# Performance work log

Measured on AMD Instinct MI355X. Metric: run time of the kernel, lower is better.

The kernel has to match this reference:

```python
import jax, jax.numpy as jnp
import numpy as np

N, E, L, F, HID, OUT = 20000, 200000, 5, 4, 128, 3


def _lin(x, w, b):
    # torch Linear convention: w is [out, in]
    return x @ w.T + b


def setup_inputs() -> dict:
    key = jax.random.key(0)
    ks = iter(jax.random.split(key, 40))
    nrm = lambda shape, s=0.05: jax.random.normal(next(ks), shape, dtype=jnp.float32) * s
    inp = {
        'x': jax.random.normal(next(ks), (N, L, F), dtype=jnp.float32),
        'edge_index': jax.random.randint(next(ks), (2, E), 0, N, dtype=jnp.int64),
        'edge_attr': jax.random.normal(next(ks), (E, F), dtype=jnp.float32),
        'batch': jnp.zeros((N,), dtype=jnp.int64),
        'node_type': jax.random.normal(next(ks), (N, 1), dtype=jnp.float32),
        # PastStateEncoder params
        'emb': nrm((L, F), 1.0),
        'conv_w': nrm((HID, 2 * F, 3)),  # Conv1d(8,128,3) OIW
        'conv_b': nrm((HID,)),
        # FusionLayer Linear(129,128)
        'fuse_w': nrm((HID, HID + 1)), 'fuse_b': nrm((HID,)),
        # gnn1 EdgeModel: Linear(2*128+4,128), Linear(128,128)
        'g1e_w1': nrm((HID, 2 * HID + F)), 'g1e_b1': nrm((HID,)),
        'g1e_w2': nrm((HID, HID)), 'g1e_b2': nrm((HID,)),
        # gnn1 NodeModel: Linear(256,128), Linear(128,128)
        'g1n_w1': nrm((HID, 2 * HID)), 'g1n_b1': nrm((HID,)),
        'g1n_w2': nrm((HID, HID)), 'g1n_b2': nrm((HID,)),
        # gnn2 EdgeModel: Linear(2*128+128,128), Linear(128,128)
        'g2e_w1': nrm((HID, 3 * HID)), 'g2e_b1': nrm((HID,)),
        'g2e_w2': nrm((HID, HID)), 'g2e_b2': nrm((HID,)),
        # gnn2 NodeModel
        'g2n_w1': nrm((HID, 2 * HID)), 'g2n_b1': nrm((HID,)),
        'g2n_w2': nrm((HID, HID)), 'g2n_b2': nrm((HID,)),
        # final_mlp: Linear(128,128), BN(128), Linear(128,3)
        'fm_w1': nrm((HID, HID)), 'fm_b1': nrm((HID,)),
        'bn_g': jnp.ones((HID,), dtype=jnp.float32), 'bn_b': jnp.zeros((HID,), dtype=jnp.float32),
        'fm_w2': nrm((OUT, HID)), 'fm_b2': nrm((OUT,)),
    }
    return inp


def _encoder(x, emb, conv_w, conv_b):
    # x: [N, L, F]; append learned positional embedding -> [N, L, 2F]
    n = x.shape[0]
    xe = jnp.concatenate([x, jnp.broadcast_to(emb[None], (n, L, F))], axis=-1)
    xc = xe.transpose(0, 2, 1)  # [N, 2F, L]
    y = jax.lax.conv_general_dilated(
        xc, conv_w, window_strides=(1,), padding=[(1, 1)],
        dimension_numbers=('NCW', 'OIW', 'NCW'))
    y = y + conv_b[None, :, None]
    return y.mean(axis=-1)  # [N, HID]


def _edge_mlp(src, dst, ea, w1, b1, w2, b2):
    h = jax.nn.relu(_lin(jnp.concatenate([src, dst, ea], axis=1), w1, b1))
    return _lin(h, w2, b2)


def _node_mlp(x_row, ea, w1, b1, w2, b2):
    h = jax.nn.relu(_lin(jnp.concatenate([x_row, ea], axis=1), w1, b1))
    return _lin(h, w2, b2)


def reference(x, edge_index, edge_attr, batch, node_type,
              emb, conv_w, conv_b, fuse_w, fuse_b,
              g1e_w1, g1e_b1, g1e_w2, g1e_b2, g1n_w1, g1n_b1, g1n_w2, g1n_b2,
              g2e_w1, g2e_b1, g2e_w2, g2e_b2, g2n_w1, g2n_b1, g2n_w2, g2n_b2,
              fm_w1, fm_b1, bn_g, bn_b, fm_w2, fm_b2):
    row, col = edge_index[0], edge_index[1]
    h = _encoder(x, emb, conv_w, conv_b)                     # [N,128]
    h = _lin(jnp.concatenate([h, node_type], axis=-1), fuse_w, fuse_b)  # [N,128]
    # gnn1 (MetaLayer: edge model then node model; node model here is per-edge)
    ea = _edge_mlp(h[row], h[col], edge_attr, g1e_w1, g1e_b1, g1e_w2, g1e_b2)  # [E,128]
    h = _node_mlp(h[row], ea, g1n_w1, g1n_b1, g1n_w2, g1n_b2)                  # [E,128]
    # gnn2 (h now lives on edges; indices < N <= E remain valid, matching torch)
    ea = _edge_mlp(h[row], h[col], ea, g2e_w1, g2e_b1, g2e_w2, g2e_b2)
    h = _node_mlp(h[row], ea, g2n_w1, g2n_b1, g2n_w2, g2n_b2)
    # final head on edge_attr: Linear -> BatchNorm1d (training stats) -> ReLU -> Linear
    z = _lin(ea, fm_w1, fm_b1)
    mu = z.mean(axis=0)
    var = z.var(axis=0)  # biased, matches torch BN normalization
    z = (z - mu) * jax.lax.rsqrt(var + 1e-5) * bn_g + bn_b
    z = jax.nn.relu(z)
    return _lin(z, fm_w2, fm_b2)  # [E,3]
```

## Files before the change

kernel.cpp:

```cpp
#include <hip/hip_runtime.h>

#define N_NODES 20000
#define N_EDGES 200000
#define HID 128
#define STR 136
#define NBLK 3125

typedef unsigned short u16;
using bf16x8 = __attribute__((ext_vector_type(8))) __bf16;
using f32x4  = __attribute__((ext_vector_type(4))) float;

__device__ __forceinline__ u16 f2bf(float f) {
  union { float f; unsigned u; } v; v.f = f;
  unsigned u = v.u;
  return (u16)((u + 0x7FFFu + ((u >> 16) & 1u)) >> 16);
}
__device__ __forceinline__ float bf2f(unsigned s) {
  union { unsigned u; float f; } v; v.u = s << 16;
  return v.f;
}
__device__ __forceinline__ bf16x8 ld8(const u16* p) { return *(const bf16x8*)p; }

__device__ __forceinline__ void zero_acc(f32x4 acc[4][2]) {
#pragma unroll
  for (int i = 0; i < 4; ++i) {
    acc[i][0] = (f32x4){0.f, 0.f, 0.f, 0.f};
    acc[i][1] = (f32x4){0.f, 0.f, 0.f, 0.f};
  }
}

template <int KSTEPS, typename AF>
__device__ __forceinline__ void wgemm(const u16* __restrict__ PW, AF afrag,
                                      f32x4 acc[4][2], int lane, int wave) {
  const u16* pb = PW + (wave * 2 * 64 + lane) * 8;
  bf16x8 b0[2], b1[2];
  b0[0] = ld8(pb);
  b1[0] = ld8(pb + 512);
#pragma unroll
  for (int ks = 0; ks < KSTEPS; ++ks) {
    const int cur = ks & 1, nxt = cur ^ 1;
    if (ks + 1 < KSTEPS) {
      b0[nxt] = ld8(pb + (ks + 1) * 4096);
      b1[nxt] = ld8(pb + (ks + 1) * 4096 + 512);
    }
#pragma unroll
    for (int mt = 0; mt < 4; ++mt) {
      bf16x8 a = afrag(ks, mt);
      acc[mt][0] = __builtin_amdgcn_mfma_f32_16x16x32_bf16(a, b0[cur], acc[mt][0], 0, 0, 0);
      acc[mt][1] = __builtin_amdgcn_mfma_f32_16x16x32_bf16(a, b1[cur], acc[mt][1], 0, 0, 0);
    }
  }
}

template <bool RELU>
__device__ __forceinline__ void epi_store(u16* buf, const f32x4 acc[4][2],
                                          const float* __restrict__ bias,
                                          int lane, int wave) {
  const int c = lane & 15, q = lane >> 4;
  const float bb0 = bias[wave * 32 + c], bb1 = bias[wave * 32 + 16 + c];
#pragma unroll
  for (int mt = 0; mt < 4; ++mt)
#pragma unroll
    for (int nt = 0; nt < 2; ++nt) {
      const float bb = nt ? bb1 : bb0;
      const int col = wave * 32 + nt * 16 + c;
#pragma unroll
      for (int r = 0; r < 4; ++r) {
        float v = acc[mt][nt][r] + bb;
        if (RELU) v = fmaxf(v, 0.f);
        buf[(mt * 16 + q * 4 + r) * STR + col] = f2bf(v);
      }
    }
}

__device__ __forceinline__ void flush_buf(const u16* buf, u16* __restrict__ gout,
                                          int e0, int tid) {
#pragma unroll
  for (int it = 0; it < 4; ++it) {
    int cid = tid + it * 256, e = cid >> 4, p = cid & 15;
    uint4 v = *(const uint4*)(buf + e * STR + p * 8);
    *(uint4*)(gout + (size_t)(e0 + e) * HID + p * 8) = v;
  }
}

__global__ void k_fold(const float* __restrict__ emb, const float* __restrict__ conv_w,
                       const float* __restrict__ conv_b, const float* __restrict__ fuse_w,
                       const float* __restrict__ fuse_b, float* __restrict__ Mt,
                       float* __restrict__ C0, float* __restrict__ Wnt) {
  __shared__ float Ash[128][21];
  int o = threadIdx.x;
  {
    float b0 = conv_b[o];
#pragma unroll
    for (int p = 0; p < 5; ++p) {
#pragma unroll
      for (int i = 0; i < 8; ++i) {
        float s = 0.f;
#pragma unroll
        for (int k = 0; k < 3; ++k) {
          int t = p + 1 - k;
          if (t >= 0 && t < 5) s += conv_w[(o * 8 + i) * 3 + k];
        }
        s *= 0.2f;
        if (i < 4) Ash[o][p * 4 + i] = s;
        else b0 += emb[p * 4 + (i - 4)] * s;
      }
    }
    Ash[o][20] = b0;
  }
  __syncthreads();
  float m[20];
#pragma unroll
  for (int qq = 0; qq < 20; ++qq) m[qq] = 0.f;
  float c0 = fuse_b[o];
  for (int j = 0; j < 128; ++j) {
    float w = fuse_w[o * 129 + j];
#pragma unroll
    for (int qq = 0; qq < 20; ++qq) m[qq] += w * Ash[j][qq];
    c0 += w * Ash[j][20];
  }
#pragma unroll
  for (int qq = 0; qq < 20; ++qq) Mt[qq * 128 + o] = m[qq];
  C0[o] = c0;
  Wnt[o] = fuse_w[o * 129 + 128];
}

struct PackArgs {
  const float* src[7];
  u16* dst[7];
  int Kin[7];
  int ksCum[8];
};

__global__ void k_pack(PackArgs pa) {
  int bk = blockIdx.x;
  int mi = 0;
  while (bk >= pa.ksCum[mi + 1]) ++mi;
  int ks = bk - pa.ksCum[mi];
  const float* W = pa.src[mi];
  u16* D = pa.dst[mi] + ks * 4096;
  int Kin = pa.Kin[mi];
#pragma unroll
  for (int t = 0; t < 16; ++t) {
    int el = t * 256 + (int)threadIdx.x;
    int j = el & 7, ln = (el >> 3) & 63, ntile = el >> 9;
    int k = ks * 32 + ((ln >> 4) << 3) + j;
    int n = ntile * 16 + (ln & 15);
    float v = (k < Kin) ? W[n * Kin + k] : 0.0f;
    D[el] = f2bf(v);
  }
}

__global__ __launch_bounds__(256) void k_encode(const float* __restrict__ x,
                                                const float* __restrict__ node_type,
                                                const float* __restrict__ Mt,
                                                const float* __restrict__ C0,
                                                const float* __restrict__ Wnt,
                                                u16* __restrict__ h2) {
  __shared__ float xs[2][20];
  int local = threadIdx.x >> 7, o = threadIdx.x & 127;
  int node = blockIdx.x * 2 + local;
  if (threadIdx.x < 40) {
    int nn = threadIdx.x / 20, qq = threadIdx.x % 20;
    xs[nn][qq] = x[(blockIdx.x * 2 + nn) * 20 + qq];
  }
  __syncthreads();
  float acc = C0[o] + Wnt[o] * node_type[node];
#pragma unroll
  for (int qq = 0; qq < 20; ++qq) acc += xs[local][qq] * Mt[qq * 128 + o];
  h2[node * HID + o] = f2bf(acc);
}

__global__ __launch_bounds__(256, 3) void k_gnn1(
    const int* __restrict__ eidx, const float* __restrict__ eattr,
    const u16* __restrict__ h2, const u16* __restrict__ pW1, const u16* __restrict__ pW2,
    const u16* __restrict__ pW3, const u16* __restrict__ pW4, const float* __restrict__ b1,
    const float* __restrict__ b2, const float* __restrict__ b3, const float* __restrict__ b4,
    u16* __restrict__ ea1, u16* __restrict__ h3) {
  __shared__ __align__(16) u16 B0[64 * STR], B1[64 * STR], B2[64 * STR];
  const int tid = threadIdx.x, lane = tid & 63, wave = tid >> 6;
  const int e0 = blockIdx.x * 64;
  const int* rowI = eidx;
  const int* colI = eidx + N_EDGES;
  const int idr = rowI[e0 + lane], idc = colI[e0 + lane];
  const u16* hrow = h2 + (size_t)idr * HID;
  const u16* hcol = h2 + (size_t)idc * HID;

#pragma unroll
  for (int it = 0; it < 8; ++it) {
    int g = wave * 8 + it;
    int p = g & 15;
    uint4 v = *(const uint4*)((g < 16 ? hrow : hcol) + p * 8);
    *(uint4*)((g < 16 ? B0 : B1) + lane * STR + p * 8) = v;
  }

  const int m = lane & 15, q = lane >> 4;
  bf16x8 ef[4];
#pragma unroll
  for (int mt = 0; mt < 4; ++mt) {
    union { u16 s[8]; uint4 u; bf16x8 v; } t;
    t.u = make_uint4(0u, 0u, 0u, 0u);
    if (q == 0) {
      float4 a = *(const float4*)(eattr + (size_t)(e0 + mt * 16 + m) * 4);
      t.s[0] = f2bf(a.x); t.s[1] = f2bf(a.y); t.s[2] = f2bf(a.z); t.s[3] = f2bf(a.w);
    }
    ef[mt] = t.v;
  }
  __syncthreads();

  const int aoff = m * STR + q * 8;
  f32x4 acc[4][2];

  zero_acc(acc);
  wgemm<9>(pW1, [&](int ks, int mt) -> bf16x8 {
    if (ks < 4) return ld8(B0 + aoff + mt * 16 * STR + ks * 32);
    if (ks < 8) return ld8(B1 + aoff + mt * 16 * STR + (ks - 4) * 32);
    return ef[mt];
  }, acc, lane, wave);
  epi_store<true>(B2, acc, b1, lane, wave);
  __syncthreads();

  zero_acc(acc);
  wgemm<4>(pW2, [&](int ks, int mt) -> bf16x8 {
    return ld8(B2 + aoff + mt * 16 * STR + ks * 32);
  }, acc, lane, wave);
  epi_store<false>(B1, acc, b2, lane, wave);
  __syncthreads();
  flush_buf(B1, ea1, e0, tid);

  if (e0 < N_NODES) {
    zero_acc(acc);
    wgemm<8>(pW3, [&](int ks, int mt) -> bf16x8 {
      if (ks < 4) return ld8(B0 + aoff + mt * 16 * STR + ks * 32);
      return ld8(B1 + aoff + mt * 16 * STR + (ks - 4) * 32);
    }, acc, lane, wave);
    epi_store<true>(B2, acc, b3, lane, wave);
    __syncthreads();
    zero_acc(acc);
    wgemm<4>(pW4, [&](int ks, int mt) -> bf16x8 {
      return ld8(B2 + aoff + mt * 16 * STR + ks * 32);
    }, acc, lane, wave);
    epi_store<false>(B0, acc, b4, lane, wave);
    __syncthreads();
    flush_buf(B0, h3, e0, tid);
  }
}

__global__ __launch_bounds__(256, 3) void k_gnn2(
    const int* __restrict__ eidx, const u16* __restrict__ h3, u16* ea1z,
    const u16* __restrict__ pW5, const u16* __restrict__ pW6, const u16* __restrict__ pW7,
    const float* __restrict__ b5, const float* __restrict__ b6, const float* __restrict__ b7,
    float* __restrict__ partials) {
  __shared__ __align__(16) u16 B0[64 * STR], B1[64 * STR], B2[64 * STR];
  const int tid = threadIdx.x, lane = tid & 63, wave = tid >> 6;
  const int e0 = blockIdx.x * 64;
  const int* rowI = eidx;
  const int* colI = eidx + N_EDGES;
  const int idr = rowI[e0 + lane], idc = colI[e0 + lane];
  const u16* hrow = h3 + (size_t)idr * HID;
  const u16* hcol = h3 + (size_t)idc * HID;

#pragma unroll
  for (int it = 0; it < 8; ++it) {
    int g = wave * 8 + it;
    int p = g & 15;
    uint4 v = *(const uint4*)((g < 16 ? hrow : hcol) + p * 8);
    *(uint4*)((g < 16 ? B0 : B1) + lane * STR + p * 8) = v;
  }
#pragma unroll
  for (int it = 0; it < 4; ++it) {
    int cid = tid + it * 256, e = cid >> 4, p = cid & 15;
    uint4 v = *(const uint4*)(ea1z + (size_t)(e0 + e) * HID + p * 8);
    *(uint4*)(B2 + e * STR + p * 8) = v;
  }
  __syncthreads();

  const int m = lane & 15, q = lane >> 4;
  const int aoff = m * STR + q * 8;
  f32x4 acc[4][2];

  zero_acc(acc);
  wgemm<12>(pW5, [&](int ks, int mt) -> bf16x8 {
    if (ks < 4) return ld8(B0 + aoff + mt * 16 * STR + ks * 32);
    if (ks < 8) return ld8(B1 + aoff + mt * 16 * STR + (ks - 4) * 32);
    return ld8(B2 + aoff + mt * 16 * STR + (ks - 8) * 32);
  }, acc, lane, wave);
  __syncthreads();
  epi_store<true>(B0, acc, b5, lane, wave);
  __syncthreads();

  zero_acc(acc);
  wgemm<4>(pW6, [&](int ks, int mt) -> bf16x8 {
    return ld8(B0 + aoff + mt * 16 * STR + ks * 32);
  }, acc, lane, wave);
  epi_store<false>(B1, acc, b6, lane, wave);
  __syncthreads();

  zero_acc(acc);
  wgemm<4>(pW7, [&](int ks, int mt) -> bf16x8 {
    return ld8(B1 + aoff + mt * 16 * STR + ks * 32);
  }, acc, lane, wave);

  {
    const int c = lane & 15;
    const float bb0 = b7[wave * 32 + c], bb1 = b7[wave * 32 + 16 + c];
    float s0 = 0.f, q0 = 0.f, s1 = 0.f, q1 = 0.f;
#pragma unroll
    for (int mt = 0; mt < 4; ++mt)
#pragma unroll
      for (int r = 0; r < 4; ++r) {
        float v0 = acc[mt][0][r] + bb0;
        float v1 = acc[mt][1][r] + bb1;
        s0 += v0; q0 += v0 * v0;
        s1 += v1; q1 += v1 * v1;
        int row = mt * 16 + q * 4 + r;
        B2[row * STR + wave * 32 + c] = f2bf(v0);
        B2[row * STR + wave * 32 + 16 + c] = f2bf(v1);
      }
    s0 += __shfl_xor(s0, 16); s0 += __shfl_xor(s0, 32);
    q0 += __shfl_xor(q0, 16); q0 += __shfl_xor(q0, 32);
    s1 += __shfl_xor(s1, 16); s1 += __shfl_xor(s1, 32);
    q1 += __shfl_xor(q1, 16); q1 += __shfl_xor(q1, 32);
    if (lane < 16) {
      int base = blockIdx.x * 256;
      partials[base + wave * 32 + lane] = s0;
      partials[base + wave * 32 + 16 + lane] = s1;
      partials[base + 128 + wave * 32 + lane] = q0;
      partials[base + 128 + wave * 32 + 16 + lane] = q1;
    }
  }
  __syncthreads();
  flush_buf(B2, ea1z, e0, tid);
}

__global__ void k_reduce(const float* __restrict__ partials, float* __restrict__ bnacc) {
  int t = threadIdx.x;
  float s = 0.f;
  for (int b = blockIdx.x; b < NBLK; b += 64) s += partials[b * 256 + t];
  atomicAdd(&bnacc[t], s);
}

__global__ void k_bnfin(const float* __restrict__ bnacc, const float* __restrict__ bn_g,
                        const float* __restrict__ bn_b, float* __restrict__ ss) {
  int t = threadIdx.x;
  float inv = 1.0f / (float)N_EDGES;
  float mu = bnacc[t] * inv;
  float var = bnacc[128 + t] * inv - mu * mu;
  float sc = bn_g[t] * rsqrtf(var + 1e-5f);
  ss[t] = sc;
  ss[128 + t] = bn_b[t] - mu * sc;
}

__global__ __launch_bounds__(256) void k_head(const u16* __restrict__ z,
                                              const float* __restrict__ ss,
                                              const float* __restrict__ w2,
                                              const float* __restrict__ b2,
                                              float* __restrict__ out) {
  __shared__ float sh_s[128], sh_h[128], sh_w0[128], sh_w1[128], sh_w2[128];
  const int tid = threadIdx.x;
  if (tid < 128) {
    sh_s[tid] = ss[tid];
    sh_h[tid] = ss[128 + tid];
    sh_w0[tid] = w2[tid];
    sh_w1[tid] = w2[128 + tid];
    sh_w2[tid] = w2[256 + tid];
  }
  __syncthreads();
  const int e = blockIdx.x * 256 + tid;
  if (e >= N_EDGES) return;
  float a0 = b2[0], a1 = b2[1], a2 = b2[2];
  const u16* zr = z + (size_t)e * HID;
#pragma unroll
  for (int p = 0; p < 16; ++p) {
    uint4 v = *(const uint4*)(zr + p * 8);
    unsigned wv[4] = {v.x, v.y, v.z, v.w};
#pragma unroll
    for (int k = 0; k < 4; ++k) {
      int ch = p * 8 + k * 2;
      float lo = bf2f(wv[k] & 0xffffu), hi = bf2f(wv[k] >> 16);
      float r0 = fmaxf(fmaf(lo, sh_s[ch], sh_h[ch]), 0.f);
      float r1 = fmaxf(fmaf(hi, sh_s[ch + 1], sh_h[ch + 1]), 0.f);
      a0 += r0 * sh_w0[ch] + r1 * sh_w0[ch + 1];
      a1 += r0 * sh_w1[ch] + r1 * sh_w1[ch + 1];
      a2 += r0 * sh_w2[ch] + r1 * sh_w2[ch + 1];
    }
  }
  out[e * 3 + 0] = a0;
  out[e * 3 + 1] = a1;
  out[e * 3 + 2] = a2;
}

extern "C" void kernel_launch(void* const* d_in, const int* in_sizes, int n_in,
                              void* d_out, int out_size, void* d_ws, size_t ws_size,
                              hipStream_t stream) {
  const float* x         = (const float*)d_in[0];
  const int* eidx        = (const int*)d_in[1];
  const float* eattr     = (const float*)d_in[2];
  const float* node_type = (const float*)d_in[4];
  const float* emb       = (const float*)d_in[5];
  const float* conv_w    = (const float*)d_in[6];
  const float* conv_b    = (const float*)d_in[7];
  const float* fuse_w    = (const float*)d_in[8];
  const float* fuse_b    = (const float*)d_in[9];
  const float* g1e_w1    = (const float*)d_in[10];
  const float* g1e_b1    = (const float*)d_in[11];
  const float* g1e_w2    = (const float*)d_in[12];
  const float* g1e_b2    = (const float*)d_in[13];
  const float* g1n_w1    = (const float*)d_in[14];
  const float* g1n_b1    = (const float*)d_in[15];
  const float* g1n_w2    = (const float*)d_in[16];
  const float* g1n_b2    = (const float*)d_in[17];
  const float* g2e_w1    = (const float*)d_in[18];
  const float* g2e_b1    = (const float*)d_in[19];
  const float* g2e_w2    = (const float*)d_in[20];
  const float* g2e_b2    = (const float*)d_in[21];
  const float* fm_w1     = (const float*)d_in[26];
  const float* fm_b1     = (const float*)d_in[27];
  const float* bn_g      = (const float*)d_in[28];
  const float* bn_b      = (const float*)d_in[29];
  const float* fm_w2     = (const float*)d_in[30];
  const float* fm_b2     = (const float*)d_in[31];
  float* out = (float*)d_out;

  char* ws = (char*)d_ws;
  size_t off = 0;
  auto take = [&](size_t bytes) {
    void* p = ws + off;
    off = (off + bytes + 255) & ~(size_t)255;
    return p;
  };
  u16* h2   = (u16*)take((size_t)N_NODES * HID * 2);
  u16* h3   = (u16*)take((size_t)20032 * HID * 2);
  u16* ea1z = (u16*)take((size_t)N_EDGES * HID * 2);
  float* Mt    = (float*)take(20 * 128 * 4);
  float* C0    = (float*)take(128 * 4);
  float* Wnt   = (float*)take(128 * 4);
  float* bnacc = (float*)take(256 * 4);
  float* bnss  = (float*)take(256 * 4);
  float* partials = (float*)take((size_t)NBLK * 256 * 4);
  u16* pW1 = (u16*)take(9 * 4096 * 2);
  u16* pW2 = (u16*)take(4 * 4096 * 2);
  u16* pW3 = (u16*)take(8 * 4096 * 2);
  u16* pW4 = (u16*)take(4 * 4096 * 2);
  u16* pW5 = (u16*)take(12 * 4096 * 2);
  u16* pW6 = (u16*)take(4 * 4096 * 2);
  u16* pW7 = (u16*)take(4 * 4096 * 2);

  hipMemsetAsync(bnacc, 0, 256 * 4, stream);
  k_fold<<<1, 128, 0, stream>>>(emb, conv_w, conv_b, fuse_w, fuse_b, Mt, C0, Wnt);

  PackArgs pa;
  const float* srcs[7] = {g1e_w1, g1e_w2, g1n_w1, g1n_w2, g2e_w1, g2e_w2, fm_w1};
  u16* dsts[7] = {pW1, pW2, pW3, pW4, pW5, pW6, pW7};
  int kins[7] = {260, 128, 256, 128, 384, 128, 128};
  int kst[7] = {9, 4, 8, 4, 12, 4, 4};
  int cum = 0;
  for (int i = 0; i < 7; ++i) {
    pa.src[i] = srcs[i]; pa.dst[i] = dsts[i]; pa.Kin[i] = kins[i];
    pa.ksCum[i] = cum; cum += kst[i];
  }
  pa.ksCum[7] = cum;
  k_pack<<<45, 256, 0, stream>>>(pa);

  k_encode<<<N_NODES / 2, 256, 0, stream>>>(x, node_type, Mt, C0, Wnt, h2);
  k_gnn1<<<NBLK, 256, 0, stream>>>(eidx, eattr, h2, pW1, pW2, pW3, pW4,
                                   g1e_b1, g1e_b2, g1n_b1, g1n_b2, ea1z, h3);
  k_gnn2<<<NBLK, 256, 0, stream>>>(eidx, h3, ea1z, pW5, pW6, pW7,
                                   g2e_b1, g2e_b2, fm_b1, partials);
  k_reduce<<<64, 256, 0, stream>>>(partials, bnacc);
  k_bnfin<<<1, 128, 0, stream>>>(bnacc, bn_g, bn_b, bnss);
  k_head<<<(N_EDGES + 255) / 256, 256, 0, stream>>>(ea1z, bnss, fm_w2, fm_b2, out);
}
```

Baseline: 288.3 us.

## Make GNN kernels persistent with register prefetch and fold final linear pair

Both GNN edge kernels become persistent: a fixed grid of 768 blocks loops over 64-edge tiles and prefetches the next tile's gathered node rows, edge attributes and indices into registers while the current tile's GEMMs run. In gnn2 the second edge-MLP linear and the head's first linear have no nonlinearity between them, so they are folded on device into one 128x128 weight. This removes one GEMM stage and one LDS round trip per tile. BN partial sums are accumulated across tiles per block, which shrinks the partials buffer and the reduce work. The cost is higher register pressure from the prefetch buffers, extra barriers per tile, and a small rounding change from the folded weight.

```diff
diff --git a/kernel.cpp b/kernel.cpp
--- a/kernel.cpp
+++ b/kernel.cpp
@@ -4,7 +4,8 @@
 #define N_EDGES 200000
 #define HID 128
 #define STR 136
-#define NBLK 3125
+#define NT 3125
+#define GPERS 768
 
 typedef unsigned short u16;
 using bf16x8 = __attribute__((ext_vector_type(8))) __bf16;
@@ -125,11 +126,26 @@
   Wnt[o] = fuse_w[o * 129 + 128];
 }
 
+__global__ void k_fold2(const float* __restrict__ w6, const float* __restrict__ b6,
+                        const float* __restrict__ w7, const float* __restrict__ b7,
+                        float* __restrict__ W67, float* __restrict__ b67) {
+  int o = blockIdx.x;
+  int k = threadIdx.x;
+  float s = 0.f;
+  for (int j = 0; j < 128; ++j) s += w7[o * 128 + j] * w6[j * 128 + k];
+  W67[o * 128 + k] = s;
+  if (k == 0) {
+    float sb = 0.f;
+    for (int j = 0; j < 128; ++j) sb += w7[o * 128 + j] * b6[j];
+    b67[o] = sb + b7[o];
+  }
+}
+
 struct PackArgs {
-  const float* src[7];
-  u16* dst[7];
-  int Kin[7];
-  int ksCum[8];
+  const float* src[6];
+  u16* dst[6];
+  int Kin[6];
+  int ksCum[7];
 };
 
 __global__ void k_pack(PackArgs pa) {
@@ -179,164 +195,221 @@
     u16* __restrict__ ea1, u16* __restrict__ h3) {
   __shared__ __align__(16) u16 B0[64 * STR], B1[64 * STR], B2[64 * STR];
   const int tid = threadIdx.x, lane = tid & 63, wave = tid >> 6;
-  const int e0 = blockIdx.x * 64;
+  const int m = lane & 15, q = lane >> 4;
+  const int aoff = m * STR + q * 8;
   const int* rowI = eidx;
   const int* colI = eidx + N_EDGES;
-  const int idr = rowI[e0 + lane], idc = colI[e0 + lane];
-  const u16* hrow = h2 + (size_t)idr * HID;
-  const u16* hcol = h2 + (size_t)idc * HID;
-
-#pragma unroll
-  for (int it = 0; it < 8; ++it) {
-    int g = wave * 8 + it;
-    int p = g & 15;
-    uint4 v = *(const uint4*)((g < 16 ? hrow : hcol) + p * 8);
-    *(uint4*)((g < 16 ? B0 : B1) + lane * STR + p * 8) = v;
-  }
-
-  const int m = lane & 15, q = lane >> 4;
-  bf16x8 ef[4];
-#pragma unroll
-  for (int mt = 0; mt < 4; ++mt) {
-    union { u16 s[8]; uint4 u; bf16x8 v; } t;
-    t.u = make_uint4(0u, 0u, 0u, 0u);
+  const int G = gridDim.x;
+
+  uint4 st[8];
+  float4 ea[4];
+  int t = blockIdx.x;
+  {
+    const int ir = rowI[t * 64 + lane], ic = colI[t * 64 + lane];
+    const u16* hr = h2 + (size_t)ir * HID;
+    const u16* hc = h2 + (size_t)ic * HID;
+#pragma unroll
+    for (int it = 0; it < 8; ++it) {
+      int g = wave * 8 + it, p = g & 15;
+      st[it] = *(const uint4*)((g < 16 ? hr : hc) + p * 8);
+    }
     if (q == 0) {
-      float4 a = *(const float4*)(eattr + (size_t)(e0 + mt * 16 + m) * 4);
-      t.s[0] = f2bf(a.x); t.s[1] = f2bf(a.y); t.s[2] = f2bf(a.z); t.s[3] = f2bf(a.w);
-    }
-    ef[mt] = t.v;
-  }
-  __syncthreads();
-
-  const int aoff = m * STR + q * 8;
+#pragma unroll
+      for (int mt = 0; mt < 4; ++mt)
+        ea[mt] = *(const float4*)(eattr + (size_t)(t * 64 + mt * 16 + m) * 4);
+    }
+  }
+
   f32x4 acc[4][2];
-
-  zero_acc(acc);
-  wgemm<9>(pW1, [&](int ks, int mt) -> bf16x8 {
-    if (ks < 4) return ld8(B0 + aoff + mt * 16 * STR + ks * 32);
-    if (ks < 8) return ld8(B1 + aoff + mt * 16 * STR + (ks - 4) * 32);
-    return ef[mt];
-  }, acc, lane, wave);
-  epi_store<true>(B2, acc, b1, lane, wave);
-  __syncthreads();
-
-  zero_acc(acc);
-  wgemm<4>(pW2, [&](int ks, int mt) -> bf16x8 {
-    return ld8(B2 + aoff + mt * 16 * STR + ks * 32);
-  }, acc, lane, wave);
-  epi_store<false>(B1, acc, b2, lane, wave);
-  __syncthreads();
-  flush_buf(B1, ea1, e0, tid);
-
-  if (e0 < N_NODES) {
+  for (; t < NT; t += G) {
+    const int e0 = t * 64;
+    const int tc = (t + G < NT) ? (t + G) : t;
+#pragma unroll
+    for (int it = 0; it < 8; ++it) {
+      int g = wave * 8 + it, p = g & 15;
+      *(uint4*)((g < 16 ? B0 : B1) + lane * STR + p * 8) = st[it];
+    }
+    bf16x8 ef[4];
+#pragma unroll
+    for (int mt = 0; mt < 4; ++mt) {
+      union { u16 s[8]; uint4 u; bf16x8 v; } tt;
+      tt.u = make_uint4(0u, 0u, 0u, 0u);
+      if (q == 0) {
+        tt.s[0] = f2bf(ea[mt].x); tt.s[1] = f2bf(ea[mt].y);
+        tt.s[2] = f2bf(ea[mt].z); tt.s[3] = f2bf(ea[mt].w);
+      }
+      ef[mt] = tt.v;
+    }
+    const int irn = rowI[tc * 64 + lane], icn = colI[tc * 64 + lane];
+    __syncthreads();
+
     zero_acc(acc);
-    wgemm<8>(pW3, [&](int ks, int mt) -> bf16x8 {
+    wgemm<9>(pW1, [&](int ks, int mt) -> bf16x8 {
       if (ks < 4) return ld8(B0 + aoff + mt * 16 * STR + ks * 32);
-      return ld8(B1 + aoff + mt * 16 * STR + (ks - 4) * 32);
+      if (ks < 8) return ld8(B1 + aoff + mt * 16 * STR + (ks - 4) * 32);
+      return ef[mt];
     }, acc, lane, wave);
-    epi_store<true>(B2, acc, b3, lane, wave);
-    __syncthreads();
+    epi_store<true>(B2, acc, b1, lane, wave);
+    if (q == 0) {
+#pragma unroll
+      for (int mt = 0; mt < 4; ++mt)
+        ea[mt] = *(const float4*)(eattr + (size_t)(tc * 64 + mt * 16 + m) * 4);
+    }
+    __syncthreads();
+
     zero_acc(acc);
-    wgemm<4>(pW4, [&](int ks, int mt) -> bf16x8 {
+    wgemm<4>(pW2, [&](int ks, int mt) -> bf16x8 {
       return ld8(B2 + aoff + mt * 16 * STR + ks * 32);
     }, acc, lane, wave);
-    epi_store<false>(B0, acc, b4, lane, wave);
-    __syncthreads();
-    flush_buf(B0, h3, e0, tid);
+    {
+      const u16* hr = h2 + (size_t)irn * HID;
+      const u16* hc = h2 + (size_t)icn * HID;
+#pragma unroll
+      for (int it = 0; it < 8; ++it) {
+        int g = wave * 8 + it, p = g & 15;
+        st[it] = *(const uint4*)((g < 16 ? hr : hc) + p * 8);
+      }
+    }
+    epi_store<false>(B1, acc, b2, lane, wave);
+    __syncthreads();
+    flush_buf(B1, ea1, e0, tid);
+
+    if (e0 < N_NODES) {
+      zero_acc(acc);
+      wgemm<8>(pW3, [&](int ks, int mt) -> bf16x8 {
+        if (ks < 4) return ld8(B0 + aoff + mt * 16 * STR + ks * 32);
+        return ld8(B1 + aoff + mt * 16 * STR + (ks - 4) * 32);
+      }, acc, lane, wave);
+      epi_store<true>(B2, acc, b3, lane, wave);
+      __syncthreads();
+      zero_acc(acc);
+      wgemm<4>(pW4, [&](int ks, int mt) -> bf16x8 {
+        return ld8(B2 + aoff + mt * 16 * STR + ks * 32);
+      }, acc, lane, wave);
+      epi_store<false>(B0, acc, b4, lane, wave);
+      __syncthreads();
+      flush_buf(B0, h3, e0, tid);
+    }
+    __syncthreads();
   }
 }
 
 __global__ __launch_bounds__(256, 3) void k_gnn2(
     const int* __restrict__ eidx, const u16* __restrict__ h3, u16* ea1z,
-    const u16* __restrict__ pW5, const u16* __restrict__ pW6, const u16* __restrict__ pW7,
-    const float* __restrict__ b5, const float* __restrict__ b6, const float* __restrict__ b7,
+    const u16* __restrict__ pW5, const u16* __restrict__ pW67,
+    const float* __restrict__ b5, const float* __restrict__ b67,
     float* __restrict__ partials) {
   __shared__ __align__(16) u16 B0[64 * STR], B1[64 * STR], B2[64 * STR];
   const int tid = threadIdx.x, lane = tid & 63, wave = tid >> 6;
-  const int e0 = blockIdx.x * 64;
+  const int m = lane & 15, q = lane >> 4;
+  const int aoff = m * STR + q * 8;
   const int* rowI = eidx;
   const int* colI = eidx + N_EDGES;
-  const int idr = rowI[e0 + lane], idc = colI[e0 + lane];
-  const u16* hrow = h3 + (size_t)idr * HID;
-  const u16* hcol = h3 + (size_t)idc * HID;
-
-#pragma unroll
-  for (int it = 0; it < 8; ++it) {
-    int g = wave * 8 + it;
-    int p = g & 15;
-    uint4 v = *(const uint4*)((g < 16 ? hrow : hcol) + p * 8);
-    *(uint4*)((g < 16 ? B0 : B1) + lane * STR + p * 8) = v;
-  }
-#pragma unroll
-  for (int it = 0; it < 4; ++it) {
-    int cid = tid + it * 256, e = cid >> 4, p = cid & 15;
-    uint4 v = *(const uint4*)(ea1z + (size_t)(e0 + e) * HID + p * 8);
-    *(uint4*)(B2 + e * STR + p * 8) = v;
-  }
-  __syncthreads();
-
-  const int m = lane & 15, q = lane >> 4;
-  const int aoff = m * STR + q * 8;
+  const int G = gridDim.x;
+
+  uint4 st[8], se[4];
+  int t = blockIdx.x;
+  {
+    const int ir = rowI[t * 64 + lane], ic = colI[t * 64 + lane];
+    const u16* hr = h3 + (size_t)ir * HID;
+    const u16* hc = h3 + (size_t)ic * HID;
+#pragma unroll
+    for (int it = 0; it < 8; ++it) {
+      int g = wave * 8 + it, p = g & 15;
+      st[it] = *(const uint4*)((g < 16 ? hr : hc) + p * 8);
+    }
+#pragma unroll
+    for (int it = 0; it < 4; ++it) {
+      int cid = tid + it * 256, e = cid >> 4, p = cid & 15;
+      se[it] = *(const uint4*)(ea1z + (size_t)(t * 64 + e) * HID + p * 8);
+    }
+  }
+
+  float bs0 = 0.f, bq0 = 0.f, bs1 = 0.f, bq1 = 0.f;
   f32x4 acc[4][2];
-
-  zero_acc(acc);
-  wgemm<12>(pW5, [&](int ks, int mt) -> bf16x8 {
-    if (ks < 4) return ld8(B0 + aoff + mt * 16 * STR + ks * 32);
-    if (ks < 8) return ld8(B1 + aoff + mt * 16 * STR + (ks - 4) * 32);
-    return ld8(B2 + aoff + mt * 16 * STR + (ks - 8) * 32);
-  }, acc, lane, wave);
-  __syncthreads();
-  epi_store<true>(B0, acc, b5, lane, wave);
-  __syncthreads();
-
-  zero_acc(acc);
-  wgemm<4>(pW6, [&](int ks, int mt) -> bf16x8 {
-    return ld8(B0 + aoff + mt * 16 * STR + ks * 32);
-  }, acc, lane, wave);
-  epi_store<false>(B1, acc, b6, lane, wave);
-  __syncthreads();
-
-  zero_acc(acc);
-  wgemm<4>(pW7, [&](int ks, int mt) -> bf16x8 {
-    return ld8(B1 + aoff + mt * 16 * STR + ks * 32);
-  }, acc, lane, wave);
-
-  {
-    const int c = lane & 15;
-    const float bb0 = b7[wave * 32 + c], bb1 = b7[wave * 32 + 16 + c];
-    float s0 = 0.f, q0 = 0.f, s1 = 0.f, q1 = 0.f;
-#pragma unroll
-    for (int mt = 0; mt < 4; ++mt)
-#pragma unroll
-      for (int r = 0; r < 4; ++r) {
-        float v0 = acc[mt][0][r] + bb0;
-        float v1 = acc[mt][1][r] + bb1;
-        s0 += v0; q0 += v0 * v0;
-        s1 += v1; q1 += v1 * v1;
-        int row = mt * 16 + q * 4 + r;
-        B2[row * STR + wave * 32 + c] = f2bf(v0);
-        B2[row * STR + wave * 32 + 16 + c] = f2bf(v1);
+  for (; t < NT; t += G) {
+    const int e0 = t * 64;
+    const int tc = (t + G < NT) ? (t + G) : t;
+#pragma unroll
+    for (int it = 0; it < 8; ++it) {
+      int g = wave * 8 + it, p = g & 15;
+      *(uint4*)((g < 16 ? B0 : B1) + lane * STR + p * 8) = st[it];
+    }
+#pragma unroll
+    for (int it = 0; it < 4; ++it) {
+      int cid = tid + it * 256, e = cid >> 4, p = cid & 15;
+      *(uint4*)(B2 + e * STR + p * 8) = se[it];
+    }
+    const int irn = rowI[tc * 64 + lane], icn = colI[tc * 64 + lane];
+    __syncthreads();
+
+    zero_acc(acc);
+    wgemm<12>(pW5, [&](int ks, int mt) -> bf16x8 {
+      if (ks < 4) return ld8(B0 + aoff + mt * 16 * STR + ks * 32);
+      if (ks < 8) return ld8(B1 + aoff + mt * 16 * STR + (ks - 4) * 32);
+      return ld8(B2 + aoff + mt * 16 * STR + (ks - 8) * 32);
+    }, acc, lane, wave);
+    __syncthreads();
+    epi_store<true>(B0, acc, b5, lane, wave);
+    {
+      const u16* hr = h3 + (size_t)irn * HID;
+      const u16* hc = h3 + (size_t)icn * HID;
+#pragma unroll
+      for (int it = 0; it < 8; ++it) {
+        int g = wave * 8 + it, p = g & 15;
+        st[it] = *(const uint4*)((g < 16 ? hr : hc) + p * 8);
       }
-    s0 += __shfl_xor(s0, 16); s0 += __shfl_xor(s0, 32);
-    q0 += __shfl_xor(q0, 16); q0 += __shfl_xor(q0, 32);
-    s1 += __shfl_xor(s1, 16); s1 += __shfl_xor(s1, 32);
-    q1 += __shfl_xor(q1, 16); q1 += __shfl_xor(q1, 32);
-    if (lane < 16) {
-      int base = blockIdx.x * 256;
-      partials[base + wave * 32 + lane] = s0;
-      partials[base + wave * 32 + 16 + lane] = s1;
-      partials[base + 128 + wave * 32 + lane] = q0;
-      partials[base + 128 + wave * 32 + 16 + lane] = q1;
-    }
-  }
-  __syncthreads();
-  flush_buf(B2, ea1z, e0, tid);
-}
-
-__global__ void k_reduce(const float* __restrict__ partials, float* __restrict__ bnacc) {
+#pragma unroll
+      for (int it = 0; it < 4; ++it) {
+        int cid = tid + it * 256, e = cid >> 4, p = cid & 15;
+        se[it] = *(const uint4*)(ea1z + (size_t)(tc * 64 + e) * HID + p * 8);
+      }
+    }
+    __syncthreads();
+
+    zero_acc(acc);
+    wgemm<4>(pW67, [&](int ks, int mt) -> bf16x8 {
+      return ld8(B0 + aoff + mt * 16 * STR + ks * 32);
+    }, acc, lane, wave);
+    {
+      const int c = lane & 15;
+      const float bb0 = b67[wave * 32 + c], bb1 = b67[wave * 32 + 16 + c];
+#pragma unroll
+      for (int mt = 0; mt < 4; ++mt)
+#pragma unroll
+        for (int r = 0; r < 4; ++r) {
+          float v0 = acc[mt][0][r] + bb0;
+          float v1 = acc[mt][1][r] + bb1;
+          bs0 += v0; bq0 += v0 * v0;
+          bs1 += v1; bq1 += v1 * v1;
+          int row = mt * 16 + q * 4 + r;
+          B2[row * STR + wave * 32 + c] = f2bf(v0);
+          B2[row * STR + wave * 32 + 16 + c] = f2bf(v1);
+        }
+    }
+    __syncthreads();
+    flush_buf(B2, ea1z, e0, tid);
+    __syncthreads();
+  }
+
+  bs0 += __shfl_xor(bs0, 16); bs0 += __shfl_xor(bs0, 32);
+  bq0 += __shfl_xor(bq0, 16); bq0 += __shfl_xor(bq0, 32);
+  bs1 += __shfl_xor(bs1, 16); bs1 += __shfl_xor(bs1, 32);
+  bq1 += __shfl_xor(bq1, 16); bq1 += __shfl_xor(bq1, 32);
+  if (lane < 16) {
+    int base = (int)blockIdx.x * 256;
+    partials[base + wave * 32 + lane] = bs0;
+    partials[base + wave * 32 + 16 + lane] = bs1;
+    partials[base + 128 + wave * 32 + lane] = bq0;
+    partials[base + 128 + wave * 32 + 16 + lane] = bq1;
+  }
+}
+
+__global__ void k_reduce(const float* __restrict__ partials, float* __restrict__ bnacc,
+                         int nrows) {
   int t = threadIdx.x;
   float s = 0.f;
-  for (int b = blockIdx.x; b < NBLK; b += 64) s += partials[b * 256 + t];
+  for (int b = blockIdx.x; b < nrows; b += 64) s += partials[b * 256 + t];
   atomicAdd(&bnacc[t], s);
 }
 
@@ -437,37 +510,39 @@
   float* Wnt   = (float*)take(128 * 4);
   float* bnacc = (float*)take(256 * 4);
   float* bnss  = (float*)take(256 * 4);
-  float* partials = (float*)take((size_t)NBLK * 256 * 4);
-  u16* pW1 = (u16*)take(9 * 4096 * 2);
-  u16* pW2 = (u16*)take(4 * 4096 * 2);
-  u16* pW3 = (u16*)take(8 * 4096 * 2);
-  u16* pW4 = (u16*)take(4 * 4096 * 2);
-  u16* pW5 = (u16*)take(12 * 4096 * 2);
-  u16* pW6 = (u16*)take(4 * 4096 * 2);
-  u16* pW7 = (u16*)take(4 * 4096 * 2);
+  float* W67f  = (float*)take(128 * 128 * 4);
+  float* b67   = (float*)take(128 * 4);
+  float* partials = (float*)take((size_t)GPERS * 256 * 4);
+  u16* pW1  = (u16*)take(9 * 4096 * 2);
+  u16* pW2  = (u16*)take(4 * 4096 * 2);
+  u16* pW3  = (u16*)take(8 * 4096 * 2);
+  u16* pW4  = (u16*)take(4 * 4096 * 2);
+  u16* pW5  = (u16*)take(12 * 4096 * 2);
+  u16* pW67 = (u16*)take(4 * 4096 * 2);
 
   hipMemsetAsync(bnacc, 0, 256 * 4, stream);
   k_fold<<<1, 128, 0, stream>>>(emb, conv_w, conv_b, fuse_w, fuse_b, Mt, C0, Wnt);
+  k_fold2<<<128, 128, 0, stream>>>(g2e_w2, g2e_b2, fm_w1, fm_b1, W67f, b67);
 
   PackArgs pa;
-  const float* srcs[7] = {g1e_w1, g1e_w2, g1n_w1, g1n_w2, g2e_w1, g2e_w2, fm_w1};
-  u16* dsts[7] = {pW1, pW2, pW3, pW4, pW5, pW6, pW7};
-  int kins[7] = {260, 128, 256, 128, 384, 128, 128};
-  int kst[7] = {9, 4, 8, 4, 12, 4, 4};
+  const float* srcs[6] = {g1e_w1, g1e_w2, g1n_w1, g1n_w2, g2e_w1, W67f};
+  u16* dsts[6] = {pW1, pW2, pW3, pW4, pW5, pW67};
+  int kins[6] = {260, 128, 256, 128, 384, 128};
+  int kst[6] = {9, 4, 8, 4, 12, 4};
   int cum = 0;
-  for (int i = 0; i < 7; ++i) {
+  for (int i = 0; i < 6; ++i) {
     pa.src[i] = srcs[i]; pa.dst[i] = dsts[i]; pa.Kin[i] = kins[i];
     pa.ksCum[i] = cum; cum += kst[i];
   }
-  pa.ksCum[7] = cum;
-  k_pack<<<45, 256, 0, stream>>>(pa);
+  pa.ksCum[6] = cum;
+  k_pack<<<41, 256, 0, stream>>>(pa);
 
   k_encode<<<N_NODES / 2, 256, 0, stream>>>(x, node_type, Mt, C0, Wnt, h2);
-  k_gnn1<<<NBLK, 256, 0, stream>>>(eidx, eattr, h2, pW1, pW2, pW3, pW4,
-                                   g1e_b1, g1e_b2, g1n_b1, g1n_b2, ea1z, h3);
-  k_gnn2<<<NBLK, 256, 0, stream>>>(eidx, h3, ea1z, pW5, pW6, pW7,
-                                   g2e_b1, g2e_b2, fm_b1, partials);
-  k_reduce<<<64, 256, 0, stream>>>(partials, bnacc);
+  k_gnn1<<<GPERS, 256, 0, stream>>>(eidx, eattr, h2, pW1, pW2, pW3, pW4,
+                                    g1e_b1, g1e_b2, g1n_b1, g1n_b2, ea1z, h3);
+  k_gnn2<<<GPERS, 256, 0, stream>>>(eidx, h3, ea1z, pW5, pW67,
+                                    g2e_b1, b67, partials);
+  k_reduce<<<64, 256, 0, stream>>>(partials, bnacc, GPERS);
   k_bnfin<<<1, 128, 0, stream>>>(bnacc, bn_g, bn_b, bnss);
   k_head<<<(N_EDGES + 255) / 256, 256, 0, stream>>>(ea1z, bnss, fm_w2, fm_b2, out);
 }
```

After: 441.0 us. 53.0% more time.

## Fold gnn2 edge second linear into head linear and cut LDS to two buffers

Applied to the files above, without the earlier changes.

Precomputes the product of fm_w1 and g2e_w2 (with a combined bias) in a new fold kernel, so k_gnn2 runs one 128x128 GEMM fewer per edge tile. Both GNN kernels now reuse two shared-memory buffers instead of three by reloading data in stages, and launch bounds are raised to 4 blocks per CU for higher occupancy. This adds extra barriers and a second gather of hrow in gnn1. The folded weight is rounded to bf16 as a single matrix, which slightly changes rounding compared with the unfolded chain.

```diff
diff --git a/kernel.cpp b/kernel.cpp
--- a/kernel.cpp
+++ b/kernel.cpp
@@ -125,11 +125,26 @@
   Wnt[o] = fuse_w[o * 129 + 128];
 }
 
+__global__ void k_fold2(const float* __restrict__ w6, const float* __restrict__ b6,
+                        const float* __restrict__ w7, const float* __restrict__ b7,
+                        float* __restrict__ W67, float* __restrict__ b67) {
+  int o = blockIdx.x;
+  int k = threadIdx.x;
+  float s = 0.f;
+  for (int j = 0; j < 128; ++j) s += w7[o * 128 + j] * w6[j * 128 + k];
+  W67[o * 128 + k] = s;
+  if (k == 0) {
+    float sb = 0.f;
+    for (int j = 0; j < 128; ++j) sb += w7[o * 128 + j] * b6[j];
+    b67[o] = sb + b7[o];
+  }
+}
+
 struct PackArgs {
-  const float* src[7];
-  u16* dst[7];
-  int Kin[7];
-  int ksCum[8];
+  const float* src[6];
+  u16* dst[6];
+  int Kin[6];
+  int ksCum[7];
 };
 
 __global__ void k_pack(PackArgs pa) {
@@ -171,15 +186,17 @@
   h2[node * HID + o] = f2bf(acc);
 }
 
-__global__ __launch_bounds__(256, 3) void k_gnn1(
+__global__ __launch_bounds__(256, 4) void k_gnn1(
     const int* __restrict__ eidx, const float* __restrict__ eattr,
     const u16* __restrict__ h2, const u16* __restrict__ pW1, const u16* __restrict__ pW2,
     const u16* __restrict__ pW3, const u16* __restrict__ pW4, const float* __restrict__ b1,
     const float* __restrict__ b2, const float* __restrict__ b3, const float* __restrict__ b4,
     u16* __restrict__ ea1, u16* __restrict__ h3) {
-  __shared__ __align__(16) u16 B0[64 * STR], B1[64 * STR], B2[64 * STR];
+  __shared__ __align__(16) u16 B0[64 * STR], B1[64 * STR];
   const int tid = threadIdx.x, lane = tid & 63, wave = tid >> 6;
   const int e0 = blockIdx.x * 64;
+  const int m = lane & 15, q = lane >> 4;
+  const int aoff = m * STR + q * 8;
   const int* rowI = eidx;
   const int* colI = eidx + N_EDGES;
   const int idr = rowI[e0 + lane], idc = colI[e0 + lane];
@@ -194,7 +211,6 @@
     *(uint4*)((g < 16 ? B0 : B1) + lane * STR + p * 8) = v;
   }
 
-  const int m = lane & 15, q = lane >> 4;
   bf16x8 ef[4];
 #pragma unroll
   for (int mt = 0; mt < 4; ++mt) {
@@ -208,37 +224,46 @@
   }
   __syncthreads();
 
-  const int aoff = m * STR + q * 8;
   f32x4 acc[4][2];
-
   zero_acc(acc);
   wgemm<9>(pW1, [&](int ks, int mt) -> bf16x8 {
     if (ks < 4) return ld8(B0 + aoff + mt * 16 * STR + ks * 32);
     if (ks < 8) return ld8(B1 + aoff + mt * 16 * STR + (ks - 4) * 32);
     return ef[mt];
   }, acc, lane, wave);
-  epi_store<true>(B2, acc, b1, lane, wave);
+  __syncthreads();
+  epi_store<true>(B1, acc, b1, lane, wave);
   __syncthreads();
 
   zero_acc(acc);
   wgemm<4>(pW2, [&](int ks, int mt) -> bf16x8 {
-    return ld8(B2 + aoff + mt * 16 * STR + ks * 32);
+    return ld8(B1 + aoff + mt * 16 * STR + ks * 32);
   }, acc, lane, wave);
-  epi_store<false>(B1, acc, b2, lane, wave);
-  __syncthreads();
-  flush_buf(B1, ea1, e0, tid);
+  epi_store<false>(B0, acc, b2, lane, wave);
+  __syncthreads();
+  flush_buf(B0, ea1, e0, tid);
 
   if (e0 < N_NODES) {
+#pragma unroll
+    for (int it = 0; it < 4; ++it) {
+      int p = wave * 4 + it;
+      uint4 v = *(const uint4*)(hrow + p * 8);
+      *(uint4*)(B1 + lane * STR + p * 8) = v;
+    }
+    __syncthreads();
+
     zero_acc(acc);
     wgemm<8>(pW3, [&](int ks, int mt) -> bf16x8 {
-      if (ks < 4) return ld8(B0 + aoff + mt * 16 * STR + ks * 32);
-      return ld8(B1 + aoff + mt * 16 * STR + (ks - 4) * 32);
+      if (ks < 4) return ld8(B1 + aoff + mt * 16 * STR + ks * 32);
+      return ld8(B0 + aoff + mt * 16 * STR + (ks - 4) * 32);
     }, acc, lane, wave);
-    epi_store<true>(B2, acc, b3, lane, wave);
     __syncthreads();
+    epi_store<true>(B1, acc, b3, lane, wave);
+    __syncthreads();
+
     zero_acc(acc);
     wgemm<4>(pW4, [&](int ks, int mt) -> bf16x8 {
-      return ld8(B2 + aoff + mt * 16 * STR + ks * 32);
+      return ld8(B1 + aoff + mt * 16 * STR + ks * 32);
     }, acc, lane, wave);
     epi_store<false>(B0, acc, b4, lane, wave);
     __syncthreads();
@@ -246,14 +271,16 @@
   }
 }
 
-__global__ __launch_bounds__(256, 3) void k_gnn2(
+__global__ __launch_bounds__(256, 4) void k_gnn2(
     const int* __restrict__ eidx, const u16* __restrict__ h3, u16* ea1z,
-    const u16* __restrict__ pW5, const u16* __restrict__ pW6, const u16* __restrict__ pW7,
-    const float* __restrict__ b5, const float* __restrict__ b6, const float* __restrict__ b7,
+    const u16* __restrict__ pW5, const u16* __restrict__ pW67,
+    const float* __restrict__ b5, const float* __restrict__ b67,
     float* __restrict__ partials) {
-  __shared__ __align__(16) u16 B0[64 * STR], B1[64 * STR], B2[64 * STR];
+  __shared__ __align__(16) u16 B0[64 * STR], B1[64 * STR];
   const int tid = threadIdx.x, lane = tid & 63, wave = tid >> 6;
   const int e0 = blockIdx.x * 64;
+  const int m = lane & 15, q = lane >> 4;
+  const int aoff = m * STR + q * 8;
   const int* rowI = eidx;
   const int* colI = eidx + N_EDGES;
   const int idr = rowI[e0 + lane], idc = colI[e0 + lane];
@@ -267,43 +294,38 @@
     uint4 v = *(const uint4*)((g < 16 ? hrow : hcol) + p * 8);
     *(uint4*)((g < 16 ? B0 : B1) + lane * STR + p * 8) = v;
   }
+  __syncthreads();
+
+  f32x4 acc[4][2];
+  zero_acc(acc);
+  wgemm<8>(pW5, [&](int ks, int mt) -> bf16x8 {
+    if (ks < 4) return ld8(B0 + aoff + mt * 16 * STR + ks * 32);
+    return ld8(B1 + aoff + mt * 16 * STR + (ks - 4) * 32);
+  }, acc, lane, wave);
+  __syncthreads();
+
 #pragma unroll
   for (int it = 0; it < 4; ++it) {
     int cid = tid + it * 256, e = cid >> 4, p = cid & 15;
     uint4 v = *(const uint4*)(ea1z + (size_t)(e0 + e) * HID + p * 8);
-    *(uint4*)(B2 + e * STR + p * 8) = v;
-  }
-  __syncthreads();
-
-  const int m = lane & 15, q = lane >> 4;
-  const int aoff = m * STR + q * 8;
-  f32x4 acc[4][2];
-
-  zero_acc(acc);
-  wgemm<12>(pW5, [&](int ks, int mt) -> bf16x8 {
-    if (ks < 4) return ld8(B0 + aoff + mt * 16 * STR + ks * 32);
-    if (ks < 8) return ld8(B1 + aoff + mt * 16 * STR + (ks - 4) * 32);
-    return ld8(B2 + aoff + mt * 16 * STR + (ks - 8) * 32);
-  }, acc, lane, wave);
-  __syncthreads();
-  epi_store<true>(B0, acc, b5, lane, wave);
-  __syncthreads();
-
-  zero_acc(acc);
-  wgemm<4>(pW6, [&](int ks, int mt) -> bf16x8 {
+    *(uint4*)(B0 + e * STR + p * 8) = v;
+  }
+  __syncthreads();
+
+  wgemm<4>(pW5 + 8 * 4096, [&](int ks, int mt) -> bf16x8 {
     return ld8(B0 + aoff + mt * 16 * STR + ks * 32);
   }, acc, lane, wave);
-  epi_store<false>(B1, acc, b6, lane, wave);
+  epi_store<true>(B1, acc, b5, lane, wave);
   __syncthreads();
 
   zero_acc(acc);
-  wgemm<4>(pW7, [&](int ks, int mt) -> bf16x8 {
+  wgemm<4>(pW67, [&](int ks, int mt) -> bf16x8 {
     return ld8(B1 + aoff + mt * 16 * STR + ks * 32);
   }, acc, lane, wave);
 
   {
     const int c = lane & 15;
-    const float bb0 = b7[wave * 32 + c], bb1 = b7[wave * 32 + 16 + c];
+    const float bb0 = b67[wave * 32 + c], bb1 = b67[wave * 32 + 16 + c];
     float s0 = 0.f, q0 = 0.f, s1 = 0.f, q1 = 0.f;
 #pragma unroll
     for (int mt = 0; mt < 4; ++mt)
@@ -314,15 +336,15 @@
         s0 += v0; q0 += v0 * v0;
         s1 += v1; q1 += v1 * v1;
         int row = mt * 16 + q * 4 + r;
-        B2[row * STR + wave * 32 + c] = f2bf(v0);
-        B2[row * STR + wave * 32 + 16 + c] = f2bf(v1);
+        B0[row * STR + wave * 32 + c] = f2bf(v0);
+        B0[row * STR + wave * 32 + 16 + c] = f2bf(v1);
       }
     s0 += __shfl_xor(s0, 16); s0 += __shfl_xor(s0, 32);
     q0 += __shfl_xor(q0, 16); q0 += __shfl_xor(q0, 32);
     s1 += __shfl_xor(s1, 16); s1 += __shfl_xor(s1, 32);
     q1 += __shfl_xor(q1, 16); q1 += __shfl_xor(q1, 32);
     if (lane < 16) {
-      int base = blockIdx.x * 256;
+      int base = (int)blockIdx.x * 256;
       partials[base + wave * 32 + lane] = s0;
       partials[base + wave * 32 + 16 + lane] = s1;
       partials[base + 128 + wave * 32 + lane] = q0;
@@ -330,13 +352,14 @@
     }
   }
   __syncthreads();
-  flush_buf(B2, ea1z, e0, tid);
-}
-
-__global__ void k_reduce(const float* __restrict__ partials, float* __restrict__ bnacc) {
+  flush_buf(B0, ea1z, e0, tid);
+}
+
+__global__ void k_reduce(const float* __restrict__ partials, float* __restrict__ bnacc,
+                         int nrows) {
   int t = threadIdx.x;
   float s = 0.f;
-  for (int b = blockIdx.x; b < NBLK; b += 64) s += partials[b * 256 + t];
+  for (int b = blockIdx.x; b < nrows; b += 64) s += partials[b * 256 + t];
   atomicAdd(&bnacc[t], s);
 }
 
@@ -437,37 +460,39 @@
   float* Wnt   = (float*)take(128 * 4);
   float* bnacc = (float*)take(256 * 4);
   float* bnss  = (float*)take(256 * 4);
+  float* W67f  = (float*)take(128 * 128 * 4);
+  float* b67   = (float*)take(128 * 4);
   float* partials = (float*)take((size_t)NBLK * 256 * 4);
-  u16* pW1 = (u16*)take(9 * 4096 * 2);
-  u16* pW2 = (u16*)take(4 * 4096 * 2);
-  u16* pW3 = (u16*)take(8 * 4096 * 2);
-  u16* pW4 = (u16*)take(4 * 4096 * 2);
-  u16* pW5 = (u16*)take(12 * 4096 * 2);
-  u16* pW6 = (u16*)take(4 * 4096 * 2);
-  u16* pW7 = (u16*)take(4 * 4096 * 2);
+  u16* pW1  = (u16*)take(9 * 4096 * 2);
+  u16* pW2  = (u16*)take(4 * 4096 * 2);
+  u16* pW3  = (u16*)take(8 * 4096 * 2);
+  u16* pW4  = (u16*)take(4 * 4096 * 2);
+  u16* pW5  = (u16*)take(12 * 4096 * 2);
+  u16* pW67 = (u16*)take(4 * 4096 * 2);
 
   hipMemsetAsync(bnacc, 0, 256 * 4, stream);
   k_fold<<<1, 128, 0, stream>>>(emb, conv_w, conv_b, fuse_w, fuse_b, Mt, C0, Wnt);
+  k_fold2<<<128, 128, 0, stream>>>(g2e_w2, g2e_b2, fm_w1, fm_b1, W67f, b67);
 
   PackArgs pa;
-  const float* srcs[7] = {g1e_w1, g1e_w2, g1n_w1, g1n_w2, g2e_w1, g2e_w2, fm_w1};
-  u16* dsts[7] = {pW1, pW2, pW3, pW4, pW5, pW6, pW7};
-  int kins[7] = {260, 128, 256, 128, 384, 128, 128};
-  int kst[7] = {9, 4, 8, 4, 12, 4, 4};
+  const float* srcs[6] = {g1e_w1, g1e_w2, g1n_w1, g1n_w2, g2e_w1, W67f};
+  u16* dsts[6] = {pW1, pW2, pW3, pW4, pW5, pW67};
+  int kins[6] = {260, 128, 256, 128, 384, 128};
+  int kst[6] = {9, 4, 8, 4, 12, 4};
   int cum = 0;
-  for (int i = 0; i < 7; ++i) {
+  for (int i = 0; i < 6; ++i) {
     pa.src[i] = srcs[i]; pa.dst[i] = dsts[i]; pa.Kin[i] = kins[i];
     pa.ksCum[i] = cum; cum += kst[i];
   }
-  pa.ksCum[7] = cum;
-  k_pack<<<45, 256, 0, stream>>>(pa);
+  pa.ksCum[6] = cum;
+  k_pack<<<41, 256, 0, stream>>>(pa);
 
   k_encode<<<N_NODES / 2, 256, 0, stream>>>(x, node_type, Mt, C0, Wnt, h2);
   k_gnn1<<<NBLK, 256, 0, stream>>>(eidx, eattr, h2, pW1, pW2, pW3, pW4,
                                    g1e_b1, g1e_b2, g1n_b1, g1n_b2, ea1z, h3);
-  k_gnn2<<<NBLK, 256, 0, stream>>>(eidx, h3, ea1z, pW5, pW6, pW7,
-                                   g2e_b1, g2e_b2, fm_b1, partials);
-  k_reduce<<<64, 256, 0, stream>>>(partials, bnacc);
+  k_gnn2<<<NBLK, 256, 0, stream>>>(eidx, h3, ea1z, pW5, pW67,
+                                   g2e_b1, b67, partials);
+  k_reduce<<<64, 256, 0, stream>>>(partials, bnacc, NBLK);
   k_bnfin<<<1, 128, 0, stream>>>(bnacc, bn_g, bn_b, bnss);
   k_head<<<(N_EDGES + 255) / 256, 256, 0, stream>>>(ea1z, bnss, fm_w2, fm_b2, out);
 }
```

Measured after the change: 276.2 us. -4.2%, faster.
